# Kernel tuning notes

Hardware: AMD Instinct MI355X
Metric: run time of the kernel (lower is better)

Reference implementation:

```python
import jax, jax.numpy as jnp
import numpy as np

KERNEL_MUL = 2.0
KERNEL_NUM = 5
EPS = 1e-6


def setup_inputs() -> dict:
    key = jax.random.key(0)
    k1, k2 = jax.random.split(key)
    source = jax.random.normal(k1, (65536, 512), dtype=jnp.float32)
    target = jax.random.normal(k2, (65536, 512), dtype=jnp.float32)
    return {"source": source, "target": target}


def reference(source, target):
    m = source.shape[0]
    m2 = m // 2
    # odd/even index pairing (static shapes)
    x_odd = source[0:m:2][:m2]   # [m2, d]
    x_even = source[1:m:2][:m2]
    y_odd = target[0:m:2][:m2]
    y_even = target[1:m:2][:m2]

    # per-pair squared L2 distances, [m2]
    dxx = jnp.sum((x_odd - x_even) ** 2, axis=-1)
    dyy = jnp.sum((y_odd - y_even) ** 2, axis=-1)
    dxy = jnp.sum((x_odd - y_even) ** 2, axis=-1)
    dyx = jnp.sum((x_even - y_odd) ** 2, axis=-1)

    # per-pair base bandwidth, then multi-bandwidth list [K, m2]
    bw = (dxx + dyy + dxy + dyx) / 4.0
    bw = bw / (KERNEL_MUL ** (KERNEL_NUM // 2))
    mults = KERNEL_MUL ** jnp.arange(KERNEL_NUM, dtype=source.dtype)  # [K]
    bws = bw[None, :] * mults[:, None] + EPS  # [K, m2]

    h = (jnp.exp(-dxx[None, :] / bws)
         + jnp.exp(-dyy[None, :] / bws)
         - jnp.exp(-dxy[None, :] / bws)
         - jnp.exp(-dyx[None, :] / bws)).sum(axis=0)  # [m2]
    return h.mean()
```

## Files before the change

### kernel.cpp

```cpp
#include <hip/hip_runtime.h>


#define D        512
#define M2       32768
#define NBLOCKS  2048
#define NTHREADS 256
#define WPB      (NTHREADS / 64)
#define NWAVES   (NBLOCKS * WPB)
#define PPW      (M2 / NWAVES)

__global__ __launch_bounds__(NTHREADS) void mmd_pairs(const float* __restrict__ src,
                                                      const float* __restrict__ tgt,
                                                      float* __restrict__ out) {
    const int lane = threadIdx.x & 63;
    const int wid  = threadIdx.x >> 6;
    const int wave = blockIdx.x * WPB + wid;

    const int   r    = lane & 3;
    const int   k    = lane >> 2;
    const float mult = (float)(1 << k);
    const float sgn  = (k < 5) ? ((r < 2) ? 1.0f : -1.0f) : 0.0f;

    float acc = 0.0f;

#pragma unroll 2
    for (int i = 0; i < PPW; ++i) {
        const int pair = wave + i * NWAVES;
        const float* xo = src + (size_t)(2 * D) * (size_t)pair;
        const float* xe = xo + D;
        const float* yo = tgt + (size_t)(2 * D) * (size_t)pair;
        const float* ye = yo + D;

        float sxx = 0.f, syy = 0.f, sxy = 0.f, syx = 0.f;

#pragma unroll
        for (int c = 0; c < 2; ++c) {
            const int idx = c * 256 + lane * 4;
            const float4 a  = *reinterpret_cast<const float4*>(xo + idx);
            const float4 b  = *reinterpret_cast<const float4*>(xe + idx);
            const float4 g  = *reinterpret_cast<const float4*>(yo + idx);
            const float4 h4 = *reinterpret_cast<const float4*>(ye + idx);
#define COMP(f)                                   \
            { float t;                            \
              t = a.f - b.f;   sxx += t * t;      \
              t = g.f - h4.f;  syy += t * t;      \
              t = a.f - h4.f;  sxy += t * t;      \
              t = b.f - g.f;   syx += t * t; }
            COMP(x) COMP(y) COMP(z) COMP(w)
#undef COMP
        }

#pragma unroll
        for (int off = 32; off > 0; off >>= 1) {
            sxx += __shfl_xor(sxx, off, 64);
            syy += __shfl_xor(syy, off, 64);
            sxy += __shfl_xor(sxy, off, 64);
            syx += __shfl_xor(syx, off, 64);
        }

        const float bw   = (sxx + syy + sxy + syx) * 0.0625f;
        const float bws  = bw * mult + 1e-6f;
        const float dsel = (r & 2) ? ((r & 1) ? syx : sxy)
                                   : ((r & 1) ? syy : sxx);
        acc += sgn * expf(-dsel / bws);
    }

#pragma unroll
    for (int off = 32; off > 0; off >>= 1) acc += __shfl_xor(acc, off, 64);

    __shared__ float red[WPB];
    if (lane == 0) red[wid] = acc;
    __syncthreads();
    if (threadIdx.x == 0) {
        float s = 0.f;
#pragma unroll
        for (int i = 0; i < WPB; ++i) s += red[i];
        atomicAdd(out, s * (1.0f / (float)M2));
    }
}

extern "C" void kernel_launch(void* const* d_in, const int* in_sizes, int n_in,
                              void* d_out, int out_size, void* d_ws, size_t ws_size,
                              hipStream_t stream) {
    const float* src = (const float*)d_in[0];
    const float* tgt = (const float*)d_in[1];
    float* out = (float*)d_out;

    hipMemsetAsync(out, 0, sizeof(float), stream);
    mmd_pairs<<<NBLOCKS, NTHREADS, 0, stream>>>(src, tgt, out);
}
```

Before: 272.2 us.

## Assign one pair per wave and replace atomics with two-pass reduction

The persistent-style loop over multiple pairs per wave is replaced by a grid with one pair per wave (8192 blocks), and occupancy is hinted via launch bounds. The global atomicAdd and memset are replaced by per-block partial sums in workspace followed by a single-block final reduction kernel. This aims to increase memory-level parallelism and remove atomic contention, at the cost of an extra kernel launch and more block scheduling overhead.

```diff
diff --git a/kernel.cpp b/kernel.cpp
--- a/kernel.cpp
+++ b/kernel.cpp
@@ -3,67 +3,59 @@
 
 #define D        512
 #define M2       32768
-#define NBLOCKS  2048
 #define NTHREADS 256
 #define WPB      (NTHREADS / 64)
-#define NWAVES   (NBLOCKS * WPB)
-#define PPW      (M2 / NWAVES)
+#define NBLOCKS  (M2 / WPB)
 
-__global__ __launch_bounds__(NTHREADS) void mmd_pairs(const float* __restrict__ src,
-                                                      const float* __restrict__ tgt,
-                                                      float* __restrict__ out) {
+__global__ __launch_bounds__(NTHREADS, 8) void mmd_pairs(const float* __restrict__ src,
+                                                         const float* __restrict__ tgt,
+                                                         float* __restrict__ partial) {
     const int lane = threadIdx.x & 63;
     const int wid  = threadIdx.x >> 6;
-    const int wave = blockIdx.x * WPB + wid;
+    const int pair = blockIdx.x * WPB + wid;
+
+    const float* xo = src + (size_t)(2 * D) * (size_t)pair;
+    const float* xe = xo + D;
+    const float* yo = tgt + (size_t)(2 * D) * (size_t)pair;
+    const float* ye = yo + D;
+
+    float sxx = 0.f, syy = 0.f, sxy = 0.f, syx = 0.f;
+
+#pragma unroll
+    for (int c = 0; c < 2; ++c) {
+        const int idx = c * 256 + lane * 4;
+        const float4 a  = *reinterpret_cast<const float4*>(xo + idx);
+        const float4 b  = *reinterpret_cast<const float4*>(xe + idx);
+        const float4 g  = *reinterpret_cast<const float4*>(yo + idx);
+        const float4 h4 = *reinterpret_cast<const float4*>(ye + idx);
+#define COMP(f)                                   \
+        { float t;                                \
+          t = a.f - b.f;   sxx += t * t;          \
+          t = g.f - h4.f;  syy += t * t;          \
+          t = a.f - h4.f;  sxy += t * t;          \
+          t = b.f - g.f;   syx += t * t; }
+        COMP(x) COMP(y) COMP(z) COMP(w)
+#undef COMP
+    }
+
+#pragma unroll
+    for (int off = 32; off > 0; off >>= 1) {
+        sxx += __shfl_xor(sxx, off, 64);
+        syy += __shfl_xor(syy, off, 64);
+        sxy += __shfl_xor(sxy, off, 64);
+        syx += __shfl_xor(syx, off, 64);
+    }
 
     const int   r    = lane & 3;
     const int   k    = lane >> 2;
     const float mult = (float)(1 << k);
     const float sgn  = (k < 5) ? ((r < 2) ? 1.0f : -1.0f) : 0.0f;
 
-    float acc = 0.0f;
-
-#pragma unroll 2
-    for (int i = 0; i < PPW; ++i) {
-        const int pair = wave + i * NWAVES;
-        const float* xo = src + (size_t)(2 * D) * (size_t)pair;
-        const float* xe = xo + D;
-        const float* yo = tgt + (size_t)(2 * D) * (size_t)pair;
-        const float* ye = yo + D;
-
-        float sxx = 0.f, syy = 0.f, sxy = 0.f, syx = 0.f;
-
-#pragma unroll
-        for (int c = 0; c < 2; ++c) {
-            const int idx = c * 256 + lane * 4;
-            const float4 a  = *reinterpret_cast<const float4*>(xo + idx);
-            const float4 b  = *reinterpret_cast<const float4*>(xe + idx);
-            const float4 g  = *reinterpret_cast<const float4*>(yo + idx);
-            const float4 h4 = *reinterpret_cast<const float4*>(ye + idx);
-#define COMP(f)                                   \
-            { float t;                            \
-              t = a.f - b.f;   sxx += t * t;      \
-              t = g.f - h4.f;  syy += t * t;      \
-              t = a.f - h4.f;  sxy += t * t;      \
-              t = b.f - g.f;   syx += t * t; }
-            COMP(x) COMP(y) COMP(z) COMP(w)
-#undef COMP
-        }
-
-#pragma unroll
-        for (int off = 32; off > 0; off >>= 1) {
-            sxx += __shfl_xor(sxx, off, 64);
-            syy += __shfl_xor(syy, off, 64);
-            sxy += __shfl_xor(sxy, off, 64);
-            syx += __shfl_xor(syx, off, 64);
-        }
-
-        const float bw   = (sxx + syy + sxy + syx) * 0.0625f;
-        const float bws  = bw * mult + 1e-6f;
-        const float dsel = (r & 2) ? ((r & 1) ? syx : sxy)
-                                   : ((r & 1) ? syy : sxx);
-        acc += sgn * expf(-dsel / bws);
-    }
+    const float bw   = (sxx + syy + sxy + syx) * 0.0625f;
+    const float bws  = bw * mult + 1e-6f;
+    const float dsel = (r & 2) ? ((r & 1) ? syx : sxy)
+                               : ((r & 1) ? syy : sxx);
+    float acc = sgn * expf(-dsel / bws);
 
 #pragma unroll
     for (int off = 32; off > 0; off >>= 1) acc += __shfl_xor(acc, off, 64);
@@ -75,8 +67,21 @@
         float s = 0.f;
 #pragma unroll
         for (int i = 0; i < WPB; ++i) s += red[i];
-        atomicAdd(out, s * (1.0f / (float)M2));
+        partial[blockIdx.x] = s;
     }
+}
+
+__global__ __launch_bounds__(256) void mmd_final(const float* __restrict__ partial,
+                                                 float* __restrict__ out) {
+    float s = 0.f;
+    for (int i = threadIdx.x; i < NBLOCKS; i += 256) s += partial[i];
+#pragma unroll
+    for (int off = 32; off > 0; off >>= 1) s += __shfl_xor(s, off, 64);
+    __shared__ float red[4];
+    if ((threadIdx.x & 63) == 0) red[threadIdx.x >> 6] = s;
+    __syncthreads();
+    if (threadIdx.x == 0)
+        out[0] = (red[0] + red[1] + red[2] + red[3]) * (1.0f / (float)M2);
 }
 
 extern "C" void kernel_launch(void* const* d_in, const int* in_sizes, int n_in,
@@ -85,7 +90,8 @@
     const float* src = (const float*)d_in[0];
     const float* tgt = (const float*)d_in[1];
     float* out = (float*)d_out;
+    float* partial = (float*)d_ws;
 
-    hipMemsetAsync(out, 0, sizeof(float), stream);
-    mmd_pairs<<<NBLOCKS, NTHREADS, 0, stream>>>(src, tgt, out);
+    mmd_pairs<<<NBLOCKS, NTHREADS, 0, stream>>>(src, tgt, partial);
+    mmd_final<<<1, 256, 0, stream>>>(partial, out);
 }
```

After: 277.2 us. No clear change (+1.8%).
